# Kernel optimization log

Hardware: AMD Instinct MI355X
Metric: run time of the kernel (lower is better)

Reference implementation:

```python
import jax, jax.numpy as jnp
import numpy as np

ALPHA = 0.0
EPSILON = 1e-4
STD = 1.0


def _T_arr(h, std):
    # T(linspace(-10,10,h), std) from the torch module
    x = jnp.linspace(-10.0, 10.0, h)
    dx = (x[-1] - x[0]) / (h - 1)
    dispx = (h % 2 - 1) / 2.0
    g = -jnp.exp(-((x - dx * dispx) ** 2) / (2.0 * std ** 2))  # -gaussian(a=1)
    g = g + jnp.max(jnp.abs(g))
    return g / jnp.max(jnp.abs(g))


def setup_inputs() -> dict:
    key = jax.random.key(0)
    k1, k2 = jax.random.split(key)
    B, H = 512, 256
    return {
        "recon": jax.random.normal(k1, (B, H), dtype=jnp.float32),
        "target": jax.random.normal(k2, (B, H), dtype=jnp.float32),
    }


def reference(recon, target):
    B, h = recon.shape
    # Batched Toeplitz: D[b, i, j] = target[b, i-j] if 0 <= i-j < h else 0
    rows = jnp.arange(2 * h - 1)[:, None]
    cols = jnp.arange(h)[None, :]
    idx = rows - cols                                  # (2h-1, h)
    valid = (idx >= 0) & (idx < h)
    D = jnp.where(valid, target[:, jnp.clip(idx, 0, h - 1)], 0.0)  # [B, 2h-1, h]

    # Normal matrix + diagonal regularization: v = DtD + diag(alpha*diag(DtD) + eps)
    DtD = jnp.einsum('bij,bik->bjk', D, D)             # [B, h, h]
    dia = jnp.diagonal(DtD, axis1=1, axis2=2)          # [B, h]
    ar = jnp.arange(h)
    A = DtD.at[:, ar, ar].add(ALPHA * dia + EPSILON)

    # pad recon to length 2h-1 (centered, left = floor((h-1)/2))
    pad_l = (h - 1) // 2
    pad_r = (h - 1) - pad_l
    rp = jnp.pad(recon, ((0, 0), (pad_l, pad_r)))      # [B, 2h-1]
    b = jnp.einsum('bij,bi->bj', D, rp)                # D^T @ padded recon

    v = jnp.linalg.solve(A, b[..., None])[..., 0]      # [B, h] matched filters

    T = _T_arr(h, STD)
    num = jnp.sqrt(jnp.sum((T[None, :] * v) ** 2, axis=1))
    den = jnp.sqrt(jnp.sum(v ** 2, axis=1))
    return jnp.sum(0.5 * num / den)                    # reduction='sum'
```

## Files before the change

### kernel.cpp

```cpp
#include <hip/hip_runtime.h>
#include <math.h>

#define H 256
#define EPS 1e-4f

template <int CTRL>
__device__ __forceinline__ float dpp0(float x) {
    return __int_as_float(
        __builtin_amdgcn_update_dpp(0, __float_as_int(x), CTRL, 0xf, 0xf, true));
}
__device__ __forceinline__ float rdlane(float x, int l) {
    return __int_as_float(__builtin_amdgcn_readlane(__float_as_int(x), l));
}
__device__ __forceinline__ float frcp_fast(float v) { return __builtin_amdgcn_rcpf(v); }
__device__ __forceinline__ float frcp_nr(float v) {
    float r = __builtin_amdgcn_rcpf(v);
    return fmaf(r, fmaf(-v, r, 1.0f), r);
}
__device__ __forceinline__ void wave_red_sum2(float& a, float& b) {
    a += dpp0<0x111>(a);  b += dpp0<0x111>(b);
    a += dpp0<0x112>(a);  b += dpp0<0x112>(b);
    a += dpp0<0x114>(a);  b += dpp0<0x114>(b);
    a += dpp0<0x118>(a);  b += dpp0<0x118>(b);
    a += dpp0<0x142>(a);  b += dpp0<0x142>(b);
    a += dpp0<0x143>(a);  b += dpp0<0x143>(b);
    a = rdlane(a, 63);
    b = rdlane(b, 63);
}

#define STEP(KF1, KF2, LN1, LN2) do {                                   \
    float g  = -sF * isB;                                               \
    float sE = fmaf(g, sF, sB);                     \
    isB = frcp_fast(sE);                                                \
    float mu = sR * isB;                                                \
    float rlF2 = rdlane(F[KF2], (LN2));                   \
    float rlB1 = rdlane(Bv[KF1], (LN1));                  \
    float rlR2 = rdlane(Rv[KF2], (LN2));                  \
    sF = fmaf(g, rlB1, rlF2);                         \
    float tB2 = fmaf(g, rlF2, rlB1);                  \
    sR = fmaf(-mu, tB2, rlR2);                        \
    sB = sE;                                                            \
    float sb0 = dpp0<0x138>(Bv[3]);                     \
    float sr0 = dpp0<0x138>(rav[3]);                                    \
    float nB0 = fmaf(g, F[0], sb0);                                     \
    float nB1 = fmaf(g, F[1], Bv[0]);                                   \
    float nB2 = fmaf(g, F[2], Bv[1]);                                   \
    float nB3 = fmaf(g, F[3], Bv[2]);                                   \
    float nF0 = fmaf(g, sb0,  F[0]);                                    \
    float nF1 = fmaf(g, Bv[0], F[1]);                                   \
    float nF2 = fmaf(g, Bv[1], F[2]);                                   \
    float nF3 = fmaf(g, Bv[2], F[3]);                                   \
    float nr0 = fmaf(g, av[0], sr0);                                    \
    float nr1 = fmaf(g, av[1], rav[0]);                                 \
    float nr2 = fmaf(g, av[2], rav[1]);                                 \
    float nr3 = fmaf(g, av[3], rav[2]);                                 \
    float na0 = fmaf(g, sr0,   av[0]);                                  \
    float na1 = fmaf(g, rav[0], av[1]);                                 \
    float na2 = fmaf(g, rav[1], av[2]);                                 \
    float na3 = fmaf(g, rav[2], av[3]);                                 \
    xv[0] = fmaf(mu, nr0, xv[0]);  Rv[0] = fmaf(-mu, nB0, Rv[0]);       \
    xv[1] = fmaf(mu, nr1, xv[1]);  Rv[1] = fmaf(-mu, nB1, Rv[1]);       \
    xv[2] = fmaf(mu, nr2, xv[2]);  Rv[2] = fmaf(-mu, nB2, Rv[2]);       \
    xv[3] = fmaf(mu, nr3, xv[3]);  Rv[3] = fmaf(-mu, nB3, Rv[3]);       \
    Bv[0]=nB0; Bv[1]=nB1; Bv[2]=nB2; Bv[3]=nB3;                         \
    F[0]=nF0; F[1]=nF1; F[2]=nF2; F[3]=nF3;                             \
    av[0]=na0; av[1]=na1; av[2]=na2; av[3]=na3;                         \
    rav[0]=nr0; rav[1]=nr1; rav[2]=nr2; rav[3]=nr3;                     \
} while (0)

__global__ __launch_bounds__(64) void awloss_batch(
        const float* __restrict__ recon,
        const float* __restrict__ target,
        float* __restrict__ losses) {
    const int b    = blockIdx.x;
    const int lane = threadIdx.x;
    const bool l0  = (lane == 0);

    __shared__ __align__(16) float tgtp[576];
    __shared__ __align__(16) float recp[576];

    const float4 tv4 = ((const float4*)(target + b * H))[lane];
    const float4 rv4 = ((const float4*)(recon  + b * H))[lane];

    #pragma unroll
    for (int c = 0; c < 9; ++c) { tgtp[c*64+lane] = 0.f; recp[c*64+lane] = 0.f; }
    __syncthreads();
    *(float4*)&tgtp[4*lane] = tv4;
    recp[127 + 4*lane + 0] = rv4.x;
    recp[127 + 4*lane + 1] = rv4.y;
    recp[127 + 4*lane + 2] = rv4.z;
    recp[127 + 4*lane + 3] = rv4.w;
    __syncthreads();

    float racc[4] = {0.f,0.f,0.f,0.f}, bacc[4] = {0.f,0.f,0.f,0.f};
    float4 W0t = *(const float4*)&tgtp[4*lane];
    float4 W0r = *(const float4*)&recp[4*lane];
    for (int m0 = 0; m0 < 256; m0 += 4) {
        float4 W1t = *(const float4*)&tgtp[m0 + 4 + 4*lane];
        float4 W1r = *(const float4*)&recp[m0 + 4 + 4*lane];
        float t0s = rdlane(W0t.x, 0);
        float t1s = rdlane(W0t.y, 0);
        float t2s = rdlane(W0t.z, 0);
        float t3s = rdlane(W0t.w, 0);
        racc[0] = fmaf(t0s, W0t.x, racc[0]); bacc[0] = fmaf(t0s, W0r.x, bacc[0]);
        racc[1] = fmaf(t0s, W0t.y, racc[1]); bacc[1] = fmaf(t0s, W0r.y, bacc[1]);
        racc[2] = fmaf(t0s, W0t.z, racc[2]); bacc[2] = fmaf(t0s, W0r.z, bacc[2]);
        racc[3] = fmaf(t0s, W0t.w, racc[3]); bacc[3] = fmaf(t0s, W0r.w, bacc[3]);
        racc[0] = fmaf(t1s, W0t.y, racc[0]); bacc[0] = fmaf(t1s, W0r.y, bacc[0]);
        racc[1] = fmaf(t1s, W0t.z, racc[1]); bacc[1] = fmaf(t1s, W0r.z, bacc[1]);
        racc[2] = fmaf(t1s, W0t.w, racc[2]); bacc[2] = fmaf(t1s, W0r.w, bacc[2]);
        racc[3] = fmaf(t1s, W1t.x, racc[3]); bacc[3] = fmaf(t1s, W1r.x, bacc[3]);
        racc[0] = fmaf(t2s, W0t.z, racc[0]); bacc[0] = fmaf(t2s, W0r.z, bacc[0]);
        racc[1] = fmaf(t2s, W0t.w, racc[1]); bacc[1] = fmaf(t2s, W0r.w, bacc[1]);
        racc[2] = fmaf(t2s, W1t.x, racc[2]); bacc[2] = fmaf(t2s, W1r.x, bacc[2]);
        racc[3] = fmaf(t2s, W1t.y, racc[3]); bacc[3] = fmaf(t2s, W1r.y, bacc[3]);
        racc[0] = fmaf(t3s, W0t.w, racc[0]); bacc[0] = fmaf(t3s, W0r.w, bacc[0]);
        racc[1] = fmaf(t3s, W1t.x, racc[1]); bacc[1] = fmaf(t3s, W1r.x, bacc[1]);
        racc[2] = fmaf(t3s, W1t.y, racc[2]); bacc[2] = fmaf(t3s, W1r.y, bacc[2]);
        racc[3] = fmaf(t3s, W1t.z, racc[3]); bacc[3] = fmaf(t3s, W1r.z, bacc[3]);
        W0t = W1t; W0r = W1r;
    }

    float t0v = rdlane(racc[0], 0) + EPS;
    float it0 = frcp_nr(t0v);
    float F[4], Bv[4], av[4], rav[4], xv[4], Rv[4];
    #pragma unroll
    for (int c = 0; c < 4; ++c) {
        float rh = racc[c] * it0;
        if (c == 0) rh = l0 ? 1.0f : rh;
        F[c] = rh; Bv[c] = rh;
    }
    float bb0 = rdlane(bacc[0], 0) * it0;
    #pragma unroll
    for (int c = 0; c < 4; ++c) {
        float bvv = bacc[c] * it0;
        Rv[c] = fmaf(-bb0, F[c], bvv);
        xv[c] = 0.f; av[c] = 0.f; rav[c] = 0.f;
    }
    if (l0) { xv[0] = bb0; av[0] = 1.0f; rav[0] = 1.0f; }

    float sF  = rdlane(F[1], 0);
    float sB  = 1.0f, isB = 1.0f;
    float sR  = rdlane(Rv[1], 0);

    for (int t = 0; t < 63; ++t) {
        STEP(1, 2, t, t);
        STEP(2, 3, t, t);
        STEP(3, 0, t, t + 1);
        STEP(0, 1, t + 1, t + 1);
    }
    STEP(1, 2, 63, 63);
    STEP(2, 3, 63, 63);
    {
        float g  = -sF * isB;
        float sE = fmaf(g, sF, sB);
        float mu = sR * frcp_fast(sE);
        float sr0 = dpp0<0x138>(rav[3]);
        xv[0] = fmaf(mu, fmaf(g, av[0], sr0),    xv[0]);
        xv[1] = fmaf(mu, fmaf(g, av[1], rav[0]), xv[1]);
        xv[2] = fmaf(mu, fmaf(g, av[2], rav[1]), xv[2]);
        xv[3] = fmaf(mu, fmaf(g, av[3], rav[2]), xv[3]);
    }

    float sT = 0.f, sV = 0.f;
    const float dxg = 20.0f / 255.0f;
    #pragma unroll
    for (int c = 0; c < 4; ++c) {
        float v  = xv[c];
        float u  = -10.0f + dxg * (float)(4*lane + c) + 0.5f * dxg;
        float Ti = 1.0f - expf(-0.5f * u * u);
        float tw = Ti * v;
        sT += tw * tw;
        sV += v * v;
    }
    wave_red_sum2(sT, sV);
    if (l0) losses[b] = 0.5f * sqrtf(sT / sV);
}

__global__ __launch_bounds__(64) void awloss_reduce(
        const float* __restrict__ losses, float* __restrict__ out) {
    int lane = threadIdx.x;
    float s = 0.f;
    #pragma unroll
    for (int c = 0; c < 8; ++c) s += losses[c * 64 + lane];
    float d = 0.f;
    wave_red_sum2(s, d);
    if (lane == 0) out[0] = s;
}

extern "C" void kernel_launch(void* const* d_in, const int* in_sizes, int n_in,
                              void* d_out, int out_size, void* d_ws, size_t ws_size,
                              hipStream_t stream) {
    const float* recon  = (const float*)d_in[0];
    const float* target = (const float*)d_in[1];
    float* losses = (float*)d_ws;
    float* out    = (float*)d_out;

    awloss_batch<<<512, 64, 0, stream>>>(recon, target, losses);
    awloss_reduce<<<1, 64, 0, stream>>>(losses, out);
}
```

Measured before the change: 31.87 us.

## Split Levinson solve into producer/consumer waves with LDS handoff of reflection coefficients

The block grows to two waves. During the correlation phase, one wave computes the target autocorrelation and the other computes the target-recon cross-correlation. In the recursion, wave 0 runs the F/B/R Levinson updates and publishes (g, mu) per step to shared memory behind a workgroup-scope atomic counter. Wave 1 spins on that counter and applies the x/a/ra updates in batches of 8, so per-wave serial work drops and the two waves run concurrently. The cost is spin-wait polling, extra LDS traffic and a cross-wave synchronisation protocol that depends on both waves being scheduled together.

```diff
diff --git a/kernel.cpp b/kernel.cpp
--- a/kernel.cpp
+++ b/kernel.cpp
@@ -28,153 +28,191 @@
     b = rdlane(b, 63);
 }
 
-#define STEP(KF1, KF2, LN1, LN2) do {                                   \
+#define PSTEP(KF1, KF2, LN1, LN2, K) do {                               \
     float g  = -sF * isB;                                               \
-    float sE = fmaf(g, sF, sB);                     \
+    float sE = fmaf(g, sF, sB);                       \
     isB = frcp_fast(sE);                                                \
     float mu = sR * isB;                                                \
+    if (l0) gmu[(K)] = make_float2(g, mu);                              \
     float rlF2 = rdlane(F[KF2], (LN2));                   \
-    float rlB1 = rdlane(Bv[KF1], (LN1));                  \
-    float rlR2 = rdlane(Rv[KF2], (LN2));                  \
-    sF = fmaf(g, rlB1, rlF2);                         \
-    float tB2 = fmaf(g, rlF2, rlB1);                  \
-    sR = fmaf(-mu, tB2, rlR2);                        \
+    float rlB1 = rdlane(B[KF1], (LN1));                   \
+    float rlR2 = rdlane(R[KF2], (LN2));                   \
+    sF = fmaf(g, rlB1, rlF2);                                           \
+    float tB2 = fmaf(g, rlF2, rlB1);                                    \
+    sR = fmaf(-mu, tB2, rlR2);                                          \
     sB = sE;                                                            \
-    float sb0 = dpp0<0x138>(Bv[3]);                     \
-    float sr0 = dpp0<0x138>(rav[3]);                                    \
+    float sb0 = dpp0<0x138>(B[3]);                      \
     float nB0 = fmaf(g, F[0], sb0);                                     \
-    float nB1 = fmaf(g, F[1], Bv[0]);                                   \
-    float nB2 = fmaf(g, F[2], Bv[1]);                                   \
-    float nB3 = fmaf(g, F[3], Bv[2]);                                   \
+    float nB1 = fmaf(g, F[1], B[0]);                                    \
+    float nB2 = fmaf(g, F[2], B[1]);                                    \
+    float nB3 = fmaf(g, F[3], B[2]);                                    \
     float nF0 = fmaf(g, sb0,  F[0]);                                    \
-    float nF1 = fmaf(g, Bv[0], F[1]);                                   \
-    float nF2 = fmaf(g, Bv[1], F[2]);                                   \
-    float nF3 = fmaf(g, Bv[2], F[3]);                                   \
-    float nr0 = fmaf(g, av[0], sr0);                                    \
-    float nr1 = fmaf(g, av[1], rav[0]);                                 \
-    float nr2 = fmaf(g, av[2], rav[1]);                                 \
-    float nr3 = fmaf(g, av[3], rav[2]);                                 \
-    float na0 = fmaf(g, sr0,   av[0]);                                  \
-    float na1 = fmaf(g, rav[0], av[1]);                                 \
-    float na2 = fmaf(g, rav[1], av[2]);                                 \
-    float na3 = fmaf(g, rav[2], av[3]);                                 \
-    xv[0] = fmaf(mu, nr0, xv[0]);  Rv[0] = fmaf(-mu, nB0, Rv[0]);       \
-    xv[1] = fmaf(mu, nr1, xv[1]);  Rv[1] = fmaf(-mu, nB1, Rv[1]);       \
-    xv[2] = fmaf(mu, nr2, xv[2]);  Rv[2] = fmaf(-mu, nB2, Rv[2]);       \
-    xv[3] = fmaf(mu, nr3, xv[3]);  Rv[3] = fmaf(-mu, nB3, Rv[3]);       \
-    Bv[0]=nB0; Bv[1]=nB1; Bv[2]=nB2; Bv[3]=nB3;                         \
+    float nF1 = fmaf(g, B[0], F[1]);                                    \
+    float nF2 = fmaf(g, B[1], F[2]);                                    \
+    float nF3 = fmaf(g, B[2], F[3]);                                    \
+    R[0] = fmaf(-mu, nB0, R[0]);                                        \
+    R[1] = fmaf(-mu, nB1, R[1]);                                        \
+    R[2] = fmaf(-mu, nB2, R[2]);                                        \
+    R[3] = fmaf(-mu, nB3, R[3]);                                        \
+    B[0]=nB0; B[1]=nB1; B[2]=nB2; B[3]=nB3;                             \
     F[0]=nF0; F[1]=nF1; F[2]=nF2; F[3]=nF3;                             \
-    av[0]=na0; av[1]=na1; av[2]=na2; av[3]=na3;                         \
-    rav[0]=nr0; rav[1]=nr1; rav[2]=nr2; rav[3]=nr3;                     \
 } while (0)
 
-__global__ __launch_bounds__(64) void awloss_batch(
+#define CSTEP(G, MU) do {                                               \
+    float g = (G), mu = (MU);                                           \
+    float sr0 = dpp0<0x138>(ra[3]);                                     \
+    float nr0 = fmaf(g, a[0], sr0);                                     \
+    float nr1 = fmaf(g, a[1], ra[0]);                                   \
+    float nr2 = fmaf(g, a[2], ra[1]);                                   \
+    float nr3 = fmaf(g, a[3], ra[2]);                                   \
+    float na0 = fmaf(g, sr0,  a[0]);                                    \
+    float na1 = fmaf(g, ra[0], a[1]);                                   \
+    float na2 = fmaf(g, ra[1], a[2]);                                   \
+    float na3 = fmaf(g, ra[2], a[3]);                                   \
+    x[0] = fmaf(mu, nr0, x[0]);                                         \
+    x[1] = fmaf(mu, nr1, x[1]);                                         \
+    x[2] = fmaf(mu, nr2, x[2]);                                         \
+    x[3] = fmaf(mu, nr3, x[3]);                                         \
+    a[0]=na0; a[1]=na1; a[2]=na2; a[3]=na3;                             \
+    ra[0]=nr0; ra[1]=nr1; ra[2]=nr2; ra[3]=nr3;                         \
+} while (0)
+
+__global__ __launch_bounds__(128) void awloss_batch(
         const float* __restrict__ recon,
         const float* __restrict__ target,
         float* __restrict__ losses) {
     const int b    = blockIdx.x;
-    const int lane = threadIdx.x;
+    const int tid  = threadIdx.x;
+    const int lane = tid & 63;
+    const int wid  = tid >> 6;
     const bool l0  = (lane == 0);
 
     __shared__ __align__(16) float tgtp[576];
     __shared__ __align__(16) float recp[576];
-
-    const float4 tv4 = ((const float4*)(target + b * H))[lane];
-    const float4 rv4 = ((const float4*)(recon  + b * H))[lane];
-
+    __shared__ __align__(16) float accR[256];
+    __shared__ __align__(16) float accBs[256];
+    __shared__ float2 gmu[256];
+    __shared__ int done;
+
+    if (tid == 0) done = -1;
     #pragma unroll
-    for (int c = 0; c < 9; ++c) { tgtp[c*64+lane] = 0.f; recp[c*64+lane] = 0.f; }
+    for (int c = 0; c < 5; ++c) {
+        int i = c * 128 + tid;
+        if (i < 576) { tgtp[i] = 0.f; recp[i] = 0.f; }
+    }
     __syncthreads();
-    *(float4*)&tgtp[4*lane] = tv4;
-    recp[127 + 4*lane + 0] = rv4.x;
-    recp[127 + 4*lane + 1] = rv4.y;
-    recp[127 + 4*lane + 2] = rv4.z;
-    recp[127 + 4*lane + 3] = rv4.w;
+    if (wid == 0) {
+        float4 tv4 = ((const float4*)(target + b * H))[lane];
+        *(float4*)&tgtp[4 * lane] = tv4;
+    } else {
+        float4 rv4 = ((const float4*)(recon + b * H))[lane];
+        recp[127 + 4*lane + 0] = rv4.x;
+        recp[127 + 4*lane + 1] = rv4.y;
+        recp[127 + 4*lane + 2] = rv4.z;
+        recp[127 + 4*lane + 3] = rv4.w;
+    }
     __syncthreads();
 
-    float racc[4] = {0.f,0.f,0.f,0.f}, bacc[4] = {0.f,0.f,0.f,0.f};
-    float4 W0t = *(const float4*)&tgtp[4*lane];
-    float4 W0r = *(const float4*)&recp[4*lane];
+    const float* W = (wid == 0) ? tgtp : recp;
+    float acc[4] = {0.f, 0.f, 0.f, 0.f};
+    float4 W0 = *(const float4*)&W[4 * lane];
     for (int m0 = 0; m0 < 256; m0 += 4) {
-        float4 W1t = *(const float4*)&tgtp[m0 + 4 + 4*lane];
-        float4 W1r = *(const float4*)&recp[m0 + 4 + 4*lane];
-        float t0s = rdlane(W0t.x, 0);
-        float t1s = rdlane(W0t.y, 0);
-        float t2s = rdlane(W0t.z, 0);
-        float t3s = rdlane(W0t.w, 0);
-        racc[0] = fmaf(t0s, W0t.x, racc[0]); bacc[0] = fmaf(t0s, W0r.x, bacc[0]);
-        racc[1] = fmaf(t0s, W0t.y, racc[1]); bacc[1] = fmaf(t0s, W0r.y, bacc[1]);
-        racc[2] = fmaf(t0s, W0t.z, racc[2]); bacc[2] = fmaf(t0s, W0r.z, bacc[2]);
-        racc[3] = fmaf(t0s, W0t.w, racc[3]); bacc[3] = fmaf(t0s, W0r.w, bacc[3]);
-        racc[0] = fmaf(t1s, W0t.y, racc[0]); bacc[0] = fmaf(t1s, W0r.y, bacc[0]);
-        racc[1] = fmaf(t1s, W0t.z, racc[1]); bacc[1] = fmaf(t1s, W0r.z, bacc[1]);
-        racc[2] = fmaf(t1s, W0t.w, racc[2]); bacc[2] = fmaf(t1s, W0r.w, bacc[2]);
-        racc[3] = fmaf(t1s, W1t.x, racc[3]); bacc[3] = fmaf(t1s, W1r.x, bacc[3]);
-        racc[0] = fmaf(t2s, W0t.z, racc[0]); bacc[0] = fmaf(t2s, W0r.z, bacc[0]);
-        racc[1] = fmaf(t2s, W0t.w, racc[1]); bacc[1] = fmaf(t2s, W0r.w, bacc[1]);
-        racc[2] = fmaf(t2s, W1t.x, racc[2]); bacc[2] = fmaf(t2s, W1r.x, bacc[2]);
-        racc[3] = fmaf(t2s, W1t.y, racc[3]); bacc[3] = fmaf(t2s, W1r.y, bacc[3]);
-        racc[0] = fmaf(t3s, W0t.w, racc[0]); bacc[0] = fmaf(t3s, W0r.w, bacc[0]);
-        racc[1] = fmaf(t3s, W1t.x, racc[1]); bacc[1] = fmaf(t3s, W1r.x, bacc[1]);
-        racc[2] = fmaf(t3s, W1t.y, racc[2]); bacc[2] = fmaf(t3s, W1r.y, bacc[2]);
-        racc[3] = fmaf(t3s, W1t.z, racc[3]); bacc[3] = fmaf(t3s, W1r.z, bacc[3]);
-        W0t = W1t; W0r = W1r;
-    }
-
-    float t0v = rdlane(racc[0], 0) + EPS;
-    float it0 = frcp_nr(t0v);
-    float F[4], Bv[4], av[4], rav[4], xv[4], Rv[4];
-    #pragma unroll
-    for (int c = 0; c < 4; ++c) {
-        float rh = racc[c] * it0;
-        if (c == 0) rh = l0 ? 1.0f : rh;
-        F[c] = rh; Bv[c] = rh;
-    }
-    float bb0 = rdlane(bacc[0], 0) * it0;
-    #pragma unroll
-    for (int c = 0; c < 4; ++c) {
-        float bvv = bacc[c] * it0;
-        Rv[c] = fmaf(-bb0, F[c], bvv);
-        xv[c] = 0.f; av[c] = 0.f; rav[c] = 0.f;
-    }
-    if (l0) { xv[0] = bb0; av[0] = 1.0f; rav[0] = 1.0f; }
-
-    float sF  = rdlane(F[1], 0);
-    float sB  = 1.0f, isB = 1.0f;
-    float sR  = rdlane(Rv[1], 0);
-
-    for (int t = 0; t < 63; ++t) {
-        STEP(1, 2, t, t);
-        STEP(2, 3, t, t);
-        STEP(3, 0, t, t + 1);
-        STEP(0, 1, t + 1, t + 1);
-    }
-    STEP(1, 2, 63, 63);
-    STEP(2, 3, 63, 63);
-    {
-        float g  = -sF * isB;
-        float sE = fmaf(g, sF, sB);
-        float mu = sR * frcp_fast(sE);
-        float sr0 = dpp0<0x138>(rav[3]);
-        xv[0] = fmaf(mu, fmaf(g, av[0], sr0),    xv[0]);
-        xv[1] = fmaf(mu, fmaf(g, av[1], rav[0]), xv[1]);
-        xv[2] = fmaf(mu, fmaf(g, av[2], rav[1]), xv[2]);
-        xv[3] = fmaf(mu, fmaf(g, av[3], rav[2]), xv[3]);
-    }
-
-    float sT = 0.f, sV = 0.f;
-    const float dxg = 20.0f / 255.0f;
-    #pragma unroll
-    for (int c = 0; c < 4; ++c) {
-        float v  = xv[c];
-        float u  = -10.0f + dxg * (float)(4*lane + c) + 0.5f * dxg;
-        float Ti = 1.0f - expf(-0.5f * u * u);
-        float tw = Ti * v;
-        sT += tw * tw;
-        sV += v * v;
-    }
-    wave_red_sum2(sT, sV);
-    if (l0) losses[b] = 0.5f * sqrtf(sT / sV);
+        float4 N  = *(const float4*)&W[m0 + 4 + 4 * lane];
+        float4 tq = *(const float4*)&tgtp[m0];
+        acc[0]=fmaf(tq.x,W0.x,acc[0]); acc[1]=fmaf(tq.x,W0.y,acc[1]);
+        acc[2]=fmaf(tq.x,W0.z,acc[2]); acc[3]=fmaf(tq.x,W0.w,acc[3]);
+        acc[0]=fmaf(tq.y,W0.y,acc[0]); acc[1]=fmaf(tq.y,W0.z,acc[1]);
+        acc[2]=fmaf(tq.y,W0.w,acc[2]); acc[3]=fmaf(tq.y,N.x ,acc[3]);
+        acc[0]=fmaf(tq.z,W0.z,acc[0]); acc[1]=fmaf(tq.z,W0.w,acc[1]);
+        acc[2]=fmaf(tq.z,N.x ,acc[2]); acc[3]=fmaf(tq.z,N.y ,acc[3]);
+        acc[0]=fmaf(tq.w,W0.w,acc[0]); acc[1]=fmaf(tq.w,N.x ,acc[1]);
+        acc[2]=fmaf(tq.w,N.y ,acc[2]); acc[3]=fmaf(tq.w,N.z ,acc[3]);
+        W0 = N;
+    }
+    if (wid == 0) *(float4*)&accR [4*lane] = make_float4(acc[0],acc[1],acc[2],acc[3]);
+    else          *(float4*)&accBs[4*lane] = make_float4(acc[0],acc[1],acc[2],acc[3]);
+    __syncthreads();
+
+    if (wid == 0) {
+        float t0v = rdlane(acc[0], 0) + EPS;
+        float it0 = frcp_nr(t0v);
+        float F[4], B[4], R[4];
+        #pragma unroll
+        for (int c = 0; c < 4; ++c) {
+            float rh = acc[c] * it0;
+            if (c == 0) rh = l0 ? 1.0f : rh;
+            F[c] = rh; B[c] = rh;
+        }
+        float4 bb4 = *(const float4*)&accBs[4 * lane];
+        float bb0 = rdlane(bb4.x, 0) * it0;
+        R[0] = fmaf(-bb0, F[0], bb4.x * it0);
+        R[1] = fmaf(-bb0, F[1], bb4.y * it0);
+        R[2] = fmaf(-bb0, F[2], bb4.z * it0);
+        R[3] = fmaf(-bb0, F[3], bb4.w * it0);
+
+        float sF  = rdlane(F[1], 0);
+        float sB  = 1.0f, isB = 1.0f;
+        float sR  = rdlane(R[1], 0);
+
+        for (int t = 0; t < 63; ++t) {
+            int k = 4 * t;
+            PSTEP(1, 2, t,     t,     k    );
+            PSTEP(2, 3, t,     t,     k + 1);
+            PSTEP(3, 0, t,     t + 1, k + 2);
+            PSTEP(0, 1, t + 1, t + 1, k + 3);
+            if (t & 1)
+                if (l0) __hip_atomic_store(&done, k + 3, __ATOMIC_RELEASE,
+                                           __HIP_MEMORY_SCOPE_WORKGROUP);
+        }
+        PSTEP(1, 2, 63, 63, 252);
+        PSTEP(2, 3, 63, 63, 253);
+        {
+            float g  = -sF * isB;
+            float sE = fmaf(g, sF, sB);
+            float mu = sR * frcp_fast(sE);
+            if (l0) gmu[254] = make_float2(g, mu);
+        }
+        if (l0) __hip_atomic_store(&done, 255, __ATOMIC_RELEASE,
+                                   __HIP_MEMORY_SCOPE_WORKGROUP);
+    } else {
+        float t0v = accR[0] + EPS;
+        float it0 = frcp_nr(t0v);
+        float bb0 = rdlane(acc[0], 0) * it0;
+        float x[4]  = {0.f,0.f,0.f,0.f};
+        float a[4]  = {0.f,0.f,0.f,0.f};
+        float ra[4] = {0.f,0.f,0.f,0.f};
+        if (l0) { x[0] = bb0; a[0] = 1.0f; ra[0] = 1.0f; }
+
+        for (int T = 0; T < 31; ++T) {
+            int tgt_step = 8 * T + 7;
+            while (__hip_atomic_load(&done, __ATOMIC_ACQUIRE,
+                                     __HIP_MEMORY_SCOPE_WORKGROUP) < tgt_step) {}
+            float2 gm8 = gmu[8 * T + (lane & 7)];
+            #pragma unroll
+            for (int s = 0; s < 8; ++s)
+                CSTEP(rdlane(gm8.x, s), rdlane(gm8.y, s));
+        }
+        while (__hip_atomic_load(&done, __ATOMIC_ACQUIRE,
+                                 __HIP_MEMORY_SCOPE_WORKGROUP) < 254) {}
+        float2 gm8 = gmu[248 + (lane & 7)];
+        #pragma unroll
+        for (int s = 0; s < 7; ++s)
+            CSTEP(rdlane(gm8.x, s), rdlane(gm8.y, s));
+
+        float sT = 0.f, sV = 0.f;
+        const float dxg = 20.0f / 255.0f;
+        #pragma unroll
+        for (int c = 0; c < 4; ++c) {
+            float v  = x[c];
+            float u  = -10.0f + dxg * (float)(4*lane + c) + 0.5f * dxg;
+            float Ti = 1.0f - expf(-0.5f * u * u);
+            float tw = Ti * v;
+            sT += tw * tw;
+            sV += v * v;
+        }
+        wave_red_sum2(sT, sV);
+        if (l0) losses[b] = 0.5f * sqrtf(sT / sV);
+    }
 }
 
 __global__ __launch_bounds__(64) void awloss_reduce(
@@ -196,6 +234,6 @@
     float* losses = (float*)d_ws;
     float* out    = (float*)d_out;
 
-    awloss_batch<<<512, 64, 0, stream>>>(recon, target, losses);
+    awloss_batch<<<512, 128, 0, stream>>>(recon, target, losses);
     awloss_reduce<<<1, 64, 0, stream>>>(losses, out);
 }
```

Result: slower. 39.62 us (+24.3%).
